# Optimization experiments

Measured on AMD Instinct MI355X. Metric: run time of the kernel, lower is better.

The kernel has to match this reference:

```python
import jax, jax.numpy as jnp
import numpy as np
from jax import lax

N_C = 1024  # number of FPS centroids (hard-coded in forward)
K = 32      # knn neighbors (hard-coded in forward)


def _fps(x, far0):
    # Faithful to the source: dist is recomputed against ONLY the latest
    # centroid each iteration (the mask/min-update in the source is dead code),
    # then far = argmax(dist).
    B = x.shape[0]
    bidx = jnp.arange(B)

    def step(far, _):
        c = x[bidx, far]                              # [B, C]
        d = jnp.sum((x - c[:, None, :]) ** 2, -1)     # [B, N]
        return jnp.argmax(d, -1), c

    _, cents = lax.scan(step, far0, None, length=N_C)  # cents: [n_c, B, C]
    return jnp.transpose(cents, (1, 0, 2))             # [B, n_c, C]


def _knn_group(x, cent):
    # squared euclidean distances (same argsort order as torch.cdist)
    d2 = (jnp.sum(cent ** 2, -1)[..., None]
          + jnp.sum(x ** 2, -1)[:, None, :]
          - 2.0 * jnp.einsum('bmc,bnc->bmn', cent, x))   # [B, n_c, N]
    _, idx = lax.top_k(-d2, K)                            # [B, n_c, K] smallest dists
    neighbors = jax.vmap(lambda xb, ib: xb[ib])(x, idx)   # [B, n_c, K, C]
    return neighbors


def _conv1x1(h, w, b):
    # 1x1 Conv1d == channel matmul; h: [B, Cin, L], w: [Cout, Cin]
    return jax.nn.relu(jnp.einsum('oi,bil->bol', w, h) + b[None, :, None])


def setup_inputs() -> dict:
    key = jax.random.key(0)
    ks = jax.random.split(key, 20)
    B, N, C = 4, 16384, 3
    num_classes = 3
    p = lambda k, shp: (jax.random.normal(k, shp, jnp.float32) * 0.02)
    return {
        'x': jax.random.normal(ks[0], (B, N, C), jnp.float32),
        'far_init': jax.random.randint(ks[1], (B,), 0, N, jnp.int32),
        'w1': p(ks[2], (64, 3)),    'b1': p(ks[3], (64,)),
        'w2': p(ks[4], (64, 64)),   'b2': p(ks[5], (64,)),
        'w3': p(ks[6], (64, 64)),   'b3': p(ks[7], (64,)),
        'w4': p(ks[8], (128, 64)),  'b4': p(ks[9], (128,)),
        'w5': p(ks[10], (1024, 128)), 'b5': p(ks[11], (1024,)),
        'fw1': p(ks[12], (512, 1024)), 'fb1': p(ks[13], (512,)),
        'fw2': p(ks[14], (256, 512)),  'fb2': p(ks[15], (256,)),
        'fw3': p(ks[16], (num_classes, 256)), 'fb3': p(ks[17], (num_classes,)),
    }


def reference(x, far_init, w1, b1, w2, b2, w3, b3, w4, b4, w5, b5,
              fw1, fb1, fw2, fb2, fw3, fb3):
    B, N, C = x.shape
    cent = _fps(x, far_init)                 # [B, n_c, C]
    neighbors = _knn_group(x, cent)          # [B, n_c, K, C]
    h = jnp.transpose(neighbors, (0, 3, 1, 2)).reshape(B, C, N_C * K)
    h = _conv1x1(h, w1, b1)
    h = _conv1x1(h, w2, b2)
    h = _conv1x1(h, w3, b3)
    h = _conv1x1(h, w4, b4)
    h = _conv1x1(h, w5, b5)                  # [B, 1024, n_c*K]
    g = jnp.max(h, axis=2)                   # global max pool -> [B, 1024]
    g = jax.nn.relu(g @ fw1.T + fb1)
    g = jax.nn.relu(g @ fw2.T + fb2)
    return g @ fw3.T + fb3                   # [B, num_classes]
```

## Files before the change

### kernel.cpp

```cpp
#include <hip/hip_runtime.h>

#define BN  4
#define NPT 16384
#define NCC 1024
#define KNN 32

#define HBINS    2048
#define CCH      4
#define CAND_CAP 768

#define OFF_CCOUNT 0
#define OFF_SCOUNT 64
#define OFF_SBITS  128
#define OFF_POOL   (128 + BN*(NPT/32)*4)
#define ZERO_BYTES (OFF_POOL + BN*NCC*4)
#define OFF_CLIST  ZERO_BYTES
#define OFF_H1     (OFF_CLIST + BN*NCC*4)
#define OFF_SLIST  (OFF_H1 + BN*512*4)

typedef short bf16x8 __attribute__((ext_vector_type(8)));
typedef float f32x4  __attribute__((ext_vector_type(4)));

__device__ __forceinline__ short f2bf(float f) {
    unsigned u = __float_as_uint(f);
    return (short)((u + 0x7fffu + ((u >> 16) & 1u)) >> 16);
}
__device__ __forceinline__ bf16x8 cvt8(const float* __restrict__ p) {
    bf16x8 v;
#pragma unroll
    for (int j = 0; j < 8; ++j) v[j] = f2bf(p[j]);
    return v;
}

__global__ __launch_bounds__(512) void fps_kernel(const float* __restrict__ x,
    const int* __restrict__ far_init, int* __restrict__ clist, int* __restrict__ ccount)
{
    const int b = blockIdx.x, t = threadIdx.x;
    __shared__ __align__(16) unsigned char seen[NPT];
    __shared__ unsigned long long slot[3];

    const float* xb = x + (size_t)b * NPT * 3;
    float px[32], py[32], pz[32];
#pragma unroll
    for (int j = 0; j < 32; ++j) {
        int idx = t + (j << 9);
        px[j] = xb[idx*3+0]; py[j] = xb[idx*3+1]; pz[j] = xb[idx*3+2];
    }
    ((uint4*)seen)[t]       = make_uint4(0,0,0,0);
    ((uint4*)seen)[t + 512] = make_uint4(0,0,0,0);
    if (t == 0) { slot[0] = 0ull; slot[1] = 0ull; slot[2] = 0ull; }
    int prev_bx = far_init[b];
    __syncthreads();
    int pbs = __builtin_amdgcn_readfirstlane(prev_bx);
    float cx = xb[pbs*3], cy = xb[pbs*3+1], cz = xb[pbs*3+2];

    int done = 0;
    for (int it = 0; it < NCC-1; ++it) {
        const int p = it % 3;
        float best = -1.0f; int bi = 0;
#pragma unroll
        for (int j = 0; j < 32; ++j) {
            float dx = __fsub_rn(px[j], cx);
            float dy = __fsub_rn(py[j], cy);
            float dz = __fsub_rn(pz[j], cz);
            float d  = __fadd_rn(__fadd_rn(__fmul_rn(dx,dx), __fmul_rn(dy,dy)),
                                 __fmul_rn(dz,dz));
            int idx = t + (j << 9);
            if (d > best) { best = d; bi = idx; }
        }
#pragma unroll
        for (int m = 1; m < 64; m <<= 1) {
            float od = __shfl_xor(best, m, 64);
            int   oi = __shfl_xor(bi,   m, 64);
            if (od > best || (od == best && oi < bi)) { best = od; bi = oi; }
        }
        if ((t & 63) == 0) {
            unsigned long long pk =
                (((unsigned long long)__float_as_uint(best)) << 32)
                | (unsigned)(NPT - 1 - bi);
            atomicMax(&slot[p], pk);
        }
        if (t == 0) seen[prev_bx] = 1;
        __syncthreads();
        int bx = NPT - 1 - (int)(unsigned)(slot[p] & 0xFFFFFFFFull);
        if (t == 0) slot[(it + 2) % 3] = 0ull;
        if (seen[bx]) { done = 1; break; }
        prev_bx = bx;
        int bxs = __builtin_amdgcn_readfirstlane(bx);
        cx = xb[bxs*3]; cy = xb[bxs*3+1]; cz = xb[bxs*3+2];
    }
    if (!done && t == 0) seen[prev_bx] = 1;
    __syncthreads();
#pragma unroll
    for (int j = 0; j < 32; ++j) {
        int idx = t + (j << 9);
        if (seen[idx]) {
            int pos = atomicAdd(&ccount[b], 1);
            clist[b * NCC + pos] = idx;
        }
    }
}

__device__ __forceinline__ unsigned key_of(float px, float py, float pz, float xn,
                                           float cx, float cy, float cz, float cn)
{
    float dot = __fadd_rn(__fadd_rn(__fmul_rn(cx,px), __fmul_rn(cy,py)), __fmul_rn(cz,pz));
    float d2  = __fsub_rn(__fadd_rn(cn, xn), __fmul_rn(2.0f, dot));
    unsigned u = __float_as_uint(d2);
    return u ^ ((u >> 31) ? 0xFFFFFFFFu : 0x80000000u);
}

__device__ __forceinline__ void wave_scan_bins(const unsigned* __restrict__ H,
    int nbins, int rem, int lane, int* __restrict__ out_bin, int* __restrict__ out_below)
{
    int per = nbins >> 6;
    int base = lane * per;
    unsigned part = 0;
    for (int q = 0; q < per; ++q) part += H[base + q];
    unsigned inc = part;
#pragma unroll
    for (int m = 1; m < 64; m <<= 1) {
        unsigned u = __shfl_up(inc, m, 64);
        if (lane >= m) inc += u;
    }
    unsigned exc = inc - part;
    unsigned long long mk = __ballot(exc < (unsigned)rem && inc >= (unsigned)rem);
    int src = __ffsll((long long)mk) - 1;
    if (lane == src) {
        unsigned run = exc; int bb = base;
        for (int q = 0; q < per; ++q) {
            unsigned h = H[base + q];
            if (run + h >= (unsigned)rem) { bb = base + q; break; }
            run += h;
        }
        *out_bin = bb; *out_below = (int)run;
    }
}

__global__ __launch_bounds__(1024) void knn_kernel(const float* __restrict__ x,
    const int* __restrict__ clist, const int* __restrict__ ccount,
    unsigned* __restrict__ sbits, int* __restrict__ slist, int* __restrict__ scount)
{
    const int b = blockIdx.y, t = threadIdx.x;
    const int lane = t & 63, w = t >> 6;
    const int cnt = ccount[b];
    const int cbase = blockIdx.x * CCH;
    if (cbase >= cnt) return;
    const int nc = min(CCH, cnt - cbase);
    const float* xb = x + (size_t)b * NPT * 3;

    __shared__ unsigned hist[CCH * HBINS];
    __shared__ unsigned cand[CCH * CAND_CAP];
    __shared__ float cpx[CCH], cpy[CCH], cpz[CCH], cpn[CCH];
    __shared__ unsigned candCnt[CCH];
    __shared__ int s_bb[CCH], s_below[CCH], s_rrem[CCH], s_need[CCH], s_pref[CCH];
    __shared__ unsigned s_tau[CCH];
    __shared__ int s_tbin, s_tbelow;

    if (t < nc) {
        int ci = clist[b * NCC + cbase + t];
        float cx = xb[ci*3], cy = xb[ci*3+1], cz = xb[ci*3+2];
        cpx[t] = cx; cpy[t] = cy; cpz[t] = cz;
        cpn[t] = __fadd_rn(__fadd_rn(__fmul_rn(cx,cx), __fmul_rn(cy,cy)), __fmul_rn(cz,cz));
        candCnt[t] = 0;
    }
    for (int i = t; i < CCH * HBINS; i += 1024) hist[i] = 0;
    __syncthreads();

    for (int j = 0; j < NPT/1024; ++j) {
        int i = t + (j << 10);
        float px = xb[i*3], py = xb[i*3+1], pz = xb[i*3+2];
        float xn = __fadd_rn(__fadd_rn(__fmul_rn(px,px), __fmul_rn(py,py)), __fmul_rn(pz,pz));
#pragma unroll
        for (int c = 0; c < CCH; ++c) {
            if (c < nc) {
                unsigned key = key_of(px,py,pz,xn, cpx[c],cpy[c],cpz[c],cpn[c]);
                atomicAdd(&hist[c*HBINS + (key >> 21)], 1u);
            }
        }
    }
    __syncthreads();

    if (w < nc)
        wave_scan_bins(&hist[w*HBINS], HBINS, KNN, lane, &s_bb[w], &s_below[w]);
    __syncthreads();
    if (t < nc) s_rrem[t] = KNN - s_below[t];
    __syncthreads();

    for (int j = 0; j < NPT/1024; ++j) {
        int i = t + (j << 10);
        float px = xb[i*3], py = xb[i*3+1], pz = xb[i*3+2];
        float xn = __fadd_rn(__fadd_rn(__fmul_rn(px,px), __fmul_rn(py,py)), __fmul_rn(pz,pz));
#pragma unroll
        for (int c = 0; c < CCH; ++c) {
            if (c < nc) {
                unsigned key = key_of(px,py,pz,xn, cpx[c],cpy[c],cpz[c],cpn[c]);
                if ((int)(key >> 21) == s_bb[c]) {
                    unsigned pos = atomicAdd(&candCnt[c], 1u);
                    if (pos < CAND_CAP) cand[c*CAND_CAP + pos] = key;
                }
            }
        }
    }
    __syncthreads();

    if (w < nc) {
        unsigned cc = candCnt[w];
        if (cc <= CAND_CAP) {
            int r = s_rrem[w] - 1;
            const unsigned* C = &cand[w*CAND_CAP];
            for (int idx = lane; idx < (int)cc; idx += 64) {
                unsigned k = C[idx]; int rank = 0;
                for (int q = 0; q < (int)cc; ++q) {
                    unsigned kq = C[q];
                    rank += (kq < k || (kq == k && q < idx)) ? 1 : 0;
                }
                if (rank == r) s_tau[w] = k;
            }
            if (lane == 0) s_need[w] = 0;
        } else if (lane == 0) s_need[w] = 1;
    }
    __syncthreads();

    for (int c = 0; c < nc; ++c) {
        if (s_need[c]) {
            const float cx = cpx[c], cy = cpy[c], cz = cpz[c], cn = cpn[c];
            for (int i = t; i < HBINS; i += 1024) hist[i] = 0;
            __syncthreads();
            for (int j = 0; j < NPT/1024; ++j) {
                int i = t + (j << 10);
                float px = xb[i*3], py = xb[i*3+1], pz = xb[i*3+2];
                float xn = __fadd_rn(__fadd_rn(__fmul_rn(px,px), __fmul_rn(py,py)), __fmul_rn(pz,pz));
                unsigned key = key_of(px,py,pz,xn, cx,cy,cz,cn);
                if ((int)(key >> 21) == s_bb[c]) atomicAdd(&hist[(key >> 10) & 2047u], 1u);
            }
            __syncthreads();
            if (w == 0) wave_scan_bins(hist, HBINS, s_rrem[c], lane, &s_tbin, &s_tbelow);
            __syncthreads();
            if (t == 0) { s_pref[c] = (s_bb[c] << 11) | s_tbin; s_rrem[c] -= s_tbelow; }
            __syncthreads();
            for (int i = t; i < 1024; i += 1024) hist[i] = 0;
            __syncthreads();
            for (int j = 0; j < NPT/1024; ++j) {
                int i = t + (j << 10);
                float px = xb[i*3], py = xb[i*3+1], pz = xb[i*3+2];
                float xn = __fadd_rn(__fadd_rn(__fmul_rn(px,px), __fmul_rn(py,py)), __fmul_rn(pz,pz));
                unsigned key = key_of(px,py,pz,xn, cx,cy,cz,cn);
                if ((int)(key >> 10) == s_pref[c]) atomicAdd(&hist[key & 1023u], 1u);
            }
            __syncthreads();
            if (w == 0) wave_scan_bins(hist, 1024, s_rrem[c], lane, &s_tbin, &s_tbelow);
            __syncthreads();
            if (t == 0) s_tau[c] = (((unsigned)s_pref[c]) << 10) | (unsigned)s_tbin;
            __syncthreads();
        }
    }
    __syncthreads();

    for (int j = 0; j < NPT/1024; ++j) {
        int i = t + (j << 10);
        float px = xb[i*3], py = xb[i*3+1], pz = xb[i*3+2];
        float xn = __fadd_rn(__fadd_rn(__fmul_rn(px,px), __fmul_rn(py,py)), __fmul_rn(pz,pz));
        bool sel = false;
#pragma unroll
        for (int c = 0; c < CCH; ++c) {
            if (c < nc) {
                unsigned key = key_of(px,py,pz,xn, cpx[c],cpy[c],cpz[c],cpn[c]);
                sel |= (key <= s_tau[c]);
            }
        }
        if (sel) {
            unsigned bit = 1u << (i & 31);
            unsigned old = atomicOr(&sbits[b*(NPT/32) + (i >> 5)], bit);
            if (!(old & bit)) {
                int pos = atomicAdd(&scount[b], 1);
                slist[b * NPT + pos] = i;
            }
        }
    }
}

#define MFMA16(a, bfr, c) __builtin_amdgcn_mfma_f32_16x16x32_bf16(a, bfr, c, 0, 0, 0)

__global__ __launch_bounds__(1024) void mlp_kernel(const float* __restrict__ x,
    const int* __restrict__ sel_list, const int* __restrict__ sel_count,
    const float* __restrict__ w1, const float* __restrict__ b1,
    const float* __restrict__ w2, const float* __restrict__ b2,
    const float* __restrict__ w3, const float* __restrict__ b3,
    const float* __restrict__ w4, const float* __restrict__ b4,
    const float* __restrict__ w5, const float* __restrict__ b5,
    float* __restrict__ pool)
{
    const int b = blockIdx.y, z = blockIdx.z, t = threadIdx.x;
    const int cnt = sel_count[b];
    if ((blockIdx.x << 6) >= cnt) return;
    const int lane = t & 63;
    const int w    = __builtin_amdgcn_readfirstlane(t >> 6);
    const int m    = lane & 15, quad = lane >> 4;

    __shared__ __align__(16) short A1[64 * 72];
    __shared__ __align__(16) short A2[64 * 72];
    __shared__ __align__(16) short A3[64 * 136];
    __shared__ float sx[3 * 64];

    const int ocA = (w >> 2) * 16 + m;
    bf16x8 bw2[2], bw3[2], bw4[2][2], bw5[4];
#pragma unroll
    for (int ks = 0; ks < 2; ++ks) {
        bw2[ks] = cvt8(w2 + ocA*64 + ks*32 + quad*8);
        bw3[ks] = cvt8(w3 + ocA*64 + ks*32 + quad*8);
    }
    int oc4i[2];
#pragma unroll
    for (int r2 = 0; r2 < 2; ++r2) {
        oc4i[r2] = ((w >> 2) + 4*r2) * 16 + m;
#pragma unroll
        for (int ks = 0; ks < 2; ++ks)
            bw4[r2][ks] = cvt8(w4 + oc4i[r2]*64 + ks*32 + quad*8);
    }
    const int oc5 = z*256 + w*16 + m;
#pragma unroll
    for (int ks = 0; ks < 4; ++ks)
        bw5[ks] = cvt8(w5 + oc5*128 + ks*32 + quad*8);
    const float bias2 = b2[ocA], bias3 = b3[ocA];
    const float bias4_0 = b4[oc4i[0]], bias4_1 = b4[oc4i[1]];
    const float bias5 = b5[oc5];
    float w1v[4][3], b1v[4];
#pragma unroll
    for (int i = 0; i < 4; ++i) {
        int oc = w*4 + i;
        w1v[i][0] = w1[oc*3+0]; w1v[i][1] = w1[oc*3+1]; w1v[i][2] = w1[oc*3+2];
        b1v[i] = b1[oc];
    }
    const int pt0 = (w & 3) * 16;

    for (int base = blockIdx.x << 6; base < cnt; base += (32 << 6)) {
        const int npts = min(64, cnt - base);
        __syncthreads();
        if (t < 64) {
            int idx = sel_list[b * NPT + base + min(t, npts - 1)];
            const float* xp = x + ((size_t)b * NPT + idx) * 3;
            sx[t] = xp[0]; sx[64 + t] = xp[1]; sx[128 + t] = xp[2];
        }
        __syncthreads();
        {
            float x0 = sx[lane], x1 = sx[64 + lane], x2 = sx[128 + lane];
#pragma unroll
            for (int i = 0; i < 4; ++i) {
                float acc = fmaf(x2, w1v[i][2], fmaf(x1, w1v[i][1],
                             fmaf(x0, w1v[i][0], b1v[i])));
                A1[lane*72 + w*4 + i] = f2bf(fmaxf(acc, 0.0f));
            }
        }
        __syncthreads();
        {
            bf16x8 a0 = *(const bf16x8*)&A1[(pt0 + m)*72 + quad*8];
            bf16x8 a1 = *(const bf16x8*)&A1[(pt0 + m)*72 + 32 + quad*8];
            f32x4 d = {0.f, 0.f, 0.f, 0.f};
            d = MFMA16(a0, bw2[0], d);
            d = MFMA16(a1, bw2[1], d);
#pragma unroll
            for (int r = 0; r < 4; ++r)
                A2[(pt0 + quad*4 + r)*72 + ocA] = f2bf(fmaxf(d[r] + bias2, 0.0f));
        }
        __syncthreads();
        {
            bf16x8 a0 = *(const bf16x8*)&A2[(pt0 + m)*72 + quad*8];
            bf16x8 a1 = *(const bf16x8*)&A2[(pt0 + m)*72 + 32 + quad*8];
            f32x4 d = {0.f, 0.f, 0.f, 0.f};
            d = MFMA16(a0, bw3[0], d);
            d = MFMA16(a1, bw3[1], d);
#pragma unroll
            for (int r = 0; r < 4; ++r)
                A1[(pt0 + quad*4 + r)*72 + ocA] = f2bf(fmaxf(d[r] + bias3, 0.0f));
        }
        __syncthreads();
        {
            bf16x8 a0 = *(const bf16x8*)&A1[(pt0 + m)*72 + quad*8];
            bf16x8 a1 = *(const bf16x8*)&A1[(pt0 + m)*72 + 32 + quad*8];
#pragma unroll
            for (int r2 = 0; r2 < 2; ++r2) {
                f32x4 d = {0.f, 0.f, 0.f, 0.f};
                d = MFMA16(a0, bw4[r2][0], d);
                d = MFMA16(a1, bw4[r2][1], d);
                float bs = r2 ? bias4_1 : bias4_0;
#pragma unroll
                for (int r = 0; r < 4; ++r)
                    A3[(pt0 + quad*4 + r)*136 + oc4i[r2]] = f2bf(fmaxf(d[r] + bs, 0.0f));
            }
        }
        __syncthreads();
        {
            float vm = 0.0f;
#pragma unroll
            for (int pt4 = 0; pt4 < 4; ++pt4) {
                const int q0 = pt4 * 16;
                f32x4 d = {0.f, 0.f, 0.f, 0.f};
#pragma unroll
                for (int ks = 0; ks < 4; ++ks) {
                    bf16x8 a = *(const bf16x8*)&A3[(q0 + m)*136 + ks*32 + quad*8];
                    d = MFMA16(a, bw5[ks], d);
                }
#pragma unroll
                for (int r = 0; r < 4; ++r)
                    vm = fmaxf(vm, fmaxf(d[r] + bias5, 0.0f));
            }
            vm = fmaxf(vm, __shfl_xor(vm, 16, 64));
            vm = fmaxf(vm, __shfl_xor(vm, 32, 64));
            if (lane < 16)
                atomicMax((int*)&pool[b*NCC + z*256 + w*16 + lane], __float_as_int(vm));
        }
    }
}

__global__ __launch_bounds__(1024) void head1_kernel(const float* __restrict__ pool,
    const float* __restrict__ fw1, const float* __restrict__ fb1,
    float* __restrict__ h1g)
{
    const int bo = blockIdx.x, b = blockIdx.y, t = threadIdx.x;
    const int lane = t & 63, w = t >> 6;
    __shared__ float g[1024];
    g[t] = pool[b*NCC + t];
    __syncthreads();
    int o = bo * 128 + w * 8;
#pragma unroll
    for (int i = 0; i < 8; ++i, ++o) {
        float acc = 0.0f;
#pragma unroll
        for (int j = 0; j < 16; ++j) {
            int k = lane + (j << 6);
            acc += g[k] * fw1[o*1024 + k];
        }
#pragma unroll
        for (int m = 1; m < 64; m <<= 1) acc += __shfl_xor(acc, m, 64);
        if (lane == 0) h1g[b*512 + o] = fmaxf(acc + fb1[o], 0.0f);
    }
}

__global__ __launch_bounds__(1024) void head2_kernel(const float* __restrict__ h1g,
    const float* __restrict__ fw2, const float* __restrict__ fb2,
    const float* __restrict__ fw3, const float* __restrict__ fb3,
    float* __restrict__ out)
{
    const int b = blockIdx.x, t = threadIdx.x;
    const int lane = t & 63, w = t >> 6;
    __shared__ float h1[512], h2[256];
    if (t < 512) h1[t] = h1g[b*512 + t];
    __syncthreads();
#pragma unroll
    for (int i = 0; i < 16; ++i) {
        int o = w * 16 + i;
        float acc = 0.0f;
#pragma unroll
        for (int j = 0; j < 8; ++j) {
            int k = lane + (j << 6);
            acc += h1[k] * fw2[o*512 + k];
        }
#pragma unroll
        for (int m = 1; m < 64; m <<= 1) acc += __shfl_xor(acc, m, 64);
        if (lane == 0) h2[o] = fmaxf(acc + fb2[o], 0.0f);
    }
    __syncthreads();
    if (w < 3) {
        float acc = 0.0f;
#pragma unroll
        for (int j = 0; j < 4; ++j) {
            int k = lane + (j << 6);
            acc += h2[k] * fw3[w*256 + k];
        }
#pragma unroll
        for (int m = 1; m < 64; m <<= 1) acc += __shfl_xor(acc, m, 64);
        if (lane == 0) out[b*3 + w] = acc + fb3[w];
    }
}

extern "C" void kernel_launch(void* const* d_in, const int* in_sizes, int n_in,
                              void* d_out, int out_size, void* d_ws, size_t ws_size,
                              hipStream_t stream)
{
    const float* x    = (const float*)d_in[0];
    const int*   far0 = (const int*)  d_in[1];
    const float *w1 = (const float*)d_in[2],  *b1 = (const float*)d_in[3];
    const float *w2 = (const float*)d_in[4],  *b2 = (const float*)d_in[5];
    const float *w3 = (const float*)d_in[6],  *b3 = (const float*)d_in[7];
    const float *w4 = (const float*)d_in[8],  *b4 = (const float*)d_in[9];
    const float *w5 = (const float*)d_in[10], *b5 = (const float*)d_in[11];
    const float *fw1 = (const float*)d_in[12], *fb1 = (const float*)d_in[13];
    const float *fw2 = (const float*)d_in[14], *fb2 = (const float*)d_in[15];
    const float *fw3 = (const float*)d_in[16], *fb3 = (const float*)d_in[17];

    char* ws = (char*)d_ws;
    int*      ccount = (int*)     (ws + OFF_CCOUNT);
    int*      scount = (int*)     (ws + OFF_SCOUNT);
    unsigned* sbits  = (unsigned*)(ws + OFF_SBITS);
    float*    pool   = (float*)   (ws + OFF_POOL);
    int*      clist  = (int*)     (ws + OFF_CLIST);
    float*    h1g    = (float*)   (ws + OFF_H1);
    int*      slist  = (int*)     (ws + OFF_SLIST);

    hipMemsetAsync(d_ws, 0, ZERO_BYTES, stream);

    fps_kernel<<<BN, 512, 0, stream>>>(x, far0, clist, ccount);
    knn_kernel<<<dim3(NCC/CCH, BN), 1024, 0, stream>>>(x, clist, ccount, sbits, slist, scount);
    mlp_kernel<<<dim3(32, BN, 4), 1024, 0, stream>>>(x, slist, scount,
        w1,b1, w2,b2, w3,b3, w4,b4, w5,b5, pool);
    head1_kernel<<<dim3(4, BN), 1024, 0, stream>>>(pool, fw1, fb1, h1g);
    head2_kernel<<<BN, 1024, 0, stream>>>(h1g, fw2,fb2, fw3,fb3, (float*)d_out);
}
```

Before: 193.0 us.

## Fold workspace zeroing into FPS kernel, pack FPS math, drop knn tail guards

Removes the separate hipMemsetAsync by having fps_kernel zero sbits, pool and the counters, which saves one launch on the stream. The FPS distance loop is rewritten with two-wide float vectors so the compiler can emit packed FP32 ops, and contraction is disabled to keep results bit-exact. knn_kernel drops the per-centroid nc guards by clamping the tail centroid index, so the unrolled loops have no branches. Duplicated centroids in a partial block only repeat work on the same points, and the sbits check keeps them from being added twice.

```diff
diff --git a/kernel.cpp b/kernel.cpp
--- a/kernel.cpp
+++ b/kernel.cpp
@@ -13,13 +13,13 @@
 #define OFF_SCOUNT 64
 #define OFF_SBITS  128
 #define OFF_POOL   (128 + BN*(NPT/32)*4)
-#define ZERO_BYTES (OFF_POOL + BN*NCC*4)
-#define OFF_CLIST  ZERO_BYTES
+#define OFF_CLIST  (OFF_POOL + BN*NCC*4)
 #define OFF_H1     (OFF_CLIST + BN*NCC*4)
 #define OFF_SLIST  (OFF_H1 + BN*512*4)
 
 typedef short bf16x8 __attribute__((ext_vector_type(8)));
 typedef float f32x4  __attribute__((ext_vector_type(4)));
+typedef float f32x2  __attribute__((ext_vector_type(2)));
 
 __device__ __forceinline__ short f2bf(float f) {
     unsigned u = __float_as_uint(f);
@@ -33,18 +33,27 @@
 }
 
 __global__ __launch_bounds__(512) void fps_kernel(const float* __restrict__ x,
-    const int* __restrict__ far_init, int* __restrict__ clist, int* __restrict__ ccount)
-{
+    const int* __restrict__ far_init, int* __restrict__ clist, int* __restrict__ ccount,
+    int* __restrict__ scount, unsigned* __restrict__ sbits, float* __restrict__ pool)
+{
+#pragma clang fp contract(off)
     const int b = blockIdx.x, t = threadIdx.x;
     __shared__ __align__(16) unsigned char seen[NPT];
     __shared__ unsigned long long slot[3];
 
+    sbits[b*(NPT/32) + t] = 0u;
+    pool[b*NCC + t] = 0.0f;
+    pool[b*NCC + 512 + t] = 0.0f;
+    if (t == 0) { ccount[b] = 0; scount[b] = 0; }
+
     const float* xb = x + (size_t)b * NPT * 3;
-    float px[32], py[32], pz[32];
-#pragma unroll
-    for (int j = 0; j < 32; ++j) {
-        int idx = t + (j << 9);
-        px[j] = xb[idx*3+0]; py[j] = xb[idx*3+1]; pz[j] = xb[idx*3+2];
+    f32x2 px[16], py[16], pz[16];
+#pragma unroll
+    for (int q = 0; q < 16; ++q) {
+        int ia = t + (q << 10), ib = ia + 512;
+        px[q] = f32x2{xb[ia*3+0], xb[ib*3+0]};
+        py[q] = f32x2{xb[ia*3+1], xb[ib*3+1]};
+        pz[q] = f32x2{xb[ia*3+2], xb[ib*3+2]};
     }
     ((uint4*)seen)[t]       = make_uint4(0,0,0,0);
     ((uint4*)seen)[t + 512] = make_uint4(0,0,0,0);
@@ -57,16 +66,20 @@
     int done = 0;
     for (int it = 0; it < NCC-1; ++it) {
         const int p = it % 3;
+        const f32x2 cX = {cx, cx}, cY = {cy, cy}, cZ = {cz, cz};
         float best = -1.0f; int bi = 0;
 #pragma unroll
-        for (int j = 0; j < 32; ++j) {
-            float dx = __fsub_rn(px[j], cx);
-            float dy = __fsub_rn(py[j], cy);
-            float dz = __fsub_rn(pz[j], cz);
-            float d  = __fadd_rn(__fadd_rn(__fmul_rn(dx,dx), __fmul_rn(dy,dy)),
-                                 __fmul_rn(dz,dz));
-            int idx = t + (j << 9);
-            if (d > best) { best = d; bi = idx; }
+        for (int q = 0; q < 16; ++q) {
+            f32x2 dx = px[q] - cX;
+            f32x2 dy = py[q] - cY;
+            f32x2 dz = pz[q] - cZ;
+            f32x2 m1 = dx * dx;
+            f32x2 m2 = dy * dy;
+            f32x2 m3 = dz * dz;
+            f32x2 s  = (m1 + m2) + m3;
+            int ia = t + (q << 10);
+            if (s.x > best) { best = s.x; bi = ia; }
+            if (s.y > best) { best = s.y; bi = ia + 512; }
         }
 #pragma unroll
         for (int m = 1; m < 64; m <<= 1) {
@@ -146,7 +159,6 @@
     const int cnt = ccount[b];
     const int cbase = blockIdx.x * CCH;
     if (cbase >= cnt) return;
-    const int nc = min(CCH, cnt - cbase);
     const float* xb = x + (size_t)b * NPT * 3;
 
     __shared__ unsigned hist[CCH * HBINS];
@@ -157,8 +169,8 @@
     __shared__ unsigned s_tau[CCH];
     __shared__ int s_tbin, s_tbelow;
 
-    if (t < nc) {
-        int ci = clist[b * NCC + cbase + t];
+    if (t < CCH) {
+        int ci = clist[b * NCC + min(cbase + t, cnt - 1)];
         float cx = xb[ci*3], cy = xb[ci*3+1], cz = xb[ci*3+2];
         cpx[t] = cx; cpy[t] = cy; cpz[t] = cz;
         cpn[t] = __fadd_rn(__fadd_rn(__fmul_rn(cx,cx), __fmul_rn(cy,cy)), __fmul_rn(cz,cz));
@@ -173,18 +185,16 @@
         float xn = __fadd_rn(__fadd_rn(__fmul_rn(px,px), __fmul_rn(py,py)), __fmul_rn(pz,pz));
 #pragma unroll
         for (int c = 0; c < CCH; ++c) {
-            if (c < nc) {
-                unsigned key = key_of(px,py,pz,xn, cpx[c],cpy[c],cpz[c],cpn[c]);
-                atomicAdd(&hist[c*HBINS + (key >> 21)], 1u);
-            }
-        }
-    }
-    __syncthreads();
-
-    if (w < nc)
+            unsigned key = key_of(px,py,pz,xn, cpx[c],cpy[c],cpz[c],cpn[c]);
+            atomicAdd(&hist[c*HBINS + (key >> 21)], 1u);
+        }
+    }
+    __syncthreads();
+
+    if (w < CCH)
         wave_scan_bins(&hist[w*HBINS], HBINS, KNN, lane, &s_bb[w], &s_below[w]);
     __syncthreads();
-    if (t < nc) s_rrem[t] = KNN - s_below[t];
+    if (t < CCH) s_rrem[t] = KNN - s_below[t];
     __syncthreads();
 
     for (int j = 0; j < NPT/1024; ++j) {
@@ -193,18 +203,16 @@
         float xn = __fadd_rn(__fadd_rn(__fmul_rn(px,px), __fmul_rn(py,py)), __fmul_rn(pz,pz));
 #pragma unroll
         for (int c = 0; c < CCH; ++c) {
-            if (c < nc) {
-                unsigned key = key_of(px,py,pz,xn, cpx[c],cpy[c],cpz[c],cpn[c]);
-                if ((int)(key >> 21) == s_bb[c]) {
-                    unsigned pos = atomicAdd(&candCnt[c], 1u);
-                    if (pos < CAND_CAP) cand[c*CAND_CAP + pos] = key;
-                }
-            }
-        }
-    }
-    __syncthreads();
-
-    if (w < nc) {
+            unsigned key = key_of(px,py,pz,xn, cpx[c],cpy[c],cpz[c],cpn[c]);
+            if ((int)(key >> 21) == s_bb[c]) {
+                unsigned pos = atomicAdd(&candCnt[c], 1u);
+                if (pos < CAND_CAP) cand[c*CAND_CAP + pos] = key;
+            }
+        }
+    }
+    __syncthreads();
+
+    if (w < CCH) {
         unsigned cc = candCnt[w];
         if (cc <= CAND_CAP) {
             int r = s_rrem[w] - 1;
@@ -222,7 +230,7 @@
     }
     __syncthreads();
 
-    for (int c = 0; c < nc; ++c) {
+    for (int c = 0; c < CCH; ++c) {
         if (s_need[c]) {
             const float cx = cpx[c], cy = cpy[c], cz = cpz[c], cn = cpn[c];
             for (int i = t; i < HBINS; i += 1024) hist[i] = 0;
@@ -264,10 +272,8 @@
         bool sel = false;
 #pragma unroll
         for (int c = 0; c < CCH; ++c) {
-            if (c < nc) {
-                unsigned key = key_of(px,py,pz,xn, cpx[c],cpy[c],cpz[c],cpn[c]);
-                sel |= (key <= s_tau[c]);
-            }
+            unsigned key = key_of(px,py,pz,xn, cpx[c],cpy[c],cpz[c],cpn[c]);
+            sel |= (key <= s_tau[c]);
         }
         if (sel) {
             unsigned bit = 1u << (i & 31);
@@ -498,9 +504,7 @@
     float*    h1g    = (float*)   (ws + OFF_H1);
     int*      slist  = (int*)     (ws + OFF_SLIST);
 
-    hipMemsetAsync(d_ws, 0, ZERO_BYTES, stream);
-
-    fps_kernel<<<BN, 512, 0, stream>>>(x, far0, clist, ccount);
+    fps_kernel<<<BN, 512, 0, stream>>>(x, far0, clist, ccount, scount, sbits, pool);
     knn_kernel<<<dim3(NCC/CCH, BN), 1024, 0, stream>>>(x, clist, ccount, sbits, slist, scount);
     mlp_kernel<<<dim3(32, BN, 4), 1024, 0, stream>>>(x, slist, scount,
         w1,b1, w2,b2, w3,b3, w4,b4, w5,b5, pool);
```

New measurement: 194.7 us. Within noise of the previous version (+0.9%).
